# Kernel tuning notes

Hardware: AMD Instinct MI355X
Metric: run time of the kernel (lower is better)

The kernel has to match this reference:

```python
import jax, jax.numpy as jnp
import numpy as np

N_NODES = 50000
N_EDGES = 800000
LATENT = 128
HIDDEN = 256
N_NODE_TYPES = 32
N_EDGE_TYPES = 8


def setup_inputs() -> dict:
    key = jax.random.key(0)
    ks = jax.random.split(key, 8)
    z = jax.random.normal(ks[0], (N_NODES, LATENT), dtype=jnp.float32)
    edge_index = jax.random.randint(ks[1], (2, N_EDGES), 0, N_NODES, dtype=jnp.int64)
    # node_type_proj: Linear(latent, num_node_types)
    s_np = 1.0 / np.sqrt(LATENT)
    W_node = jax.random.uniform(ks[2], (LATENT, N_NODE_TYPES), minval=-s_np, maxval=s_np, dtype=jnp.float32)
    b_node = jax.random.uniform(ks[3], (N_NODE_TYPES,), minval=-s_np, maxval=s_np, dtype=jnp.float32)
    # edge_mlp: Linear(2*latent, hidden) -> ReLU -> Linear(hidden, num_edge_types)
    s1 = 1.0 / np.sqrt(2 * LATENT)
    W1 = jax.random.uniform(ks[4], (2 * LATENT, HIDDEN), minval=-s1, maxval=s1, dtype=jnp.float32)
    b1 = jax.random.uniform(ks[5], (HIDDEN,), minval=-s1, maxval=s1, dtype=jnp.float32)
    s2 = 1.0 / np.sqrt(HIDDEN)
    W2 = jax.random.uniform(ks[6], (HIDDEN, N_EDGE_TYPES), minval=-s2, maxval=s2, dtype=jnp.float32)
    b2 = jax.random.uniform(ks[7], (N_EDGE_TYPES,), minval=-s2, maxval=s2, dtype=jnp.float32)
    return {"z": z, "edge_index": edge_index, "W_node": W_node, "b_node": b_node,
            "W1": W1, "b1": b1, "W2": W2, "b2": b2}


def reference(z, edge_index, W_node, b_node, W1, b1, W2, b2):
    # node logits: [N, num_node_types]
    node_logits = z @ W_node + b_node
    row, col = edge_index[0], edge_index[1]
    # gather node pairs and concat: [E, 2*latent]
    edge_features = jnp.concatenate([z[row], z[col]], axis=-1)
    h = jax.nn.relu(edge_features @ W1 + b1)
    edge_logits = h @ W2 + b2  # [E, num_edge_types]
    return (node_logits, edge_logits)
```

## Files before the change

### kernel.cpp

```cpp
#include <hip/hip_runtime.h>
#include <hip/hip_bf16.h>
#include <stdint.h>

#define NNODES 50000
#define NEDGES 800000
#define LATENT 128
#define NTYPES 32
#define NTILES 25000
#define GRID_E 512

typedef __bf16 bf16x8 __attribute__((ext_vector_type(8)));
typedef float floatx4 __attribute__((ext_vector_type(4)));
typedef unsigned int u32;

#if defined(__has_builtin)
#if __has_builtin(__builtin_amdgcn_global_load_lds)
#define HAS_GLD_LDS 1
#endif
#endif

__device__ __forceinline__ void lds_barrier() {
    asm volatile("s_waitcnt lgkmcnt(0)\n\ts_barrier" ::: "memory");
}

__device__ __forceinline__ void gather16(const __hip_bfloat16* g, __hip_bfloat16* lbase, int lane) {
#ifdef HAS_GLD_LDS
    __builtin_amdgcn_global_load_lds(
        (const __attribute__((address_space(1))) u32*)(uintptr_t)g,
        (__attribute__((address_space(3))) u32*)(u32)(uintptr_t)lbase,
        16, 0, 0);
#else
    *(uint4*)(lbase + lane * 8) = *(const uint4*)g;
#endif
}

__device__ __forceinline__ int load_idx(const int* ei, bool i64, int half, size_t e) {
    size_t pos = (size_t)half * NEDGES + e;
    return i64 ? ei[2 * pos] : ei[pos];
}

__global__ __launch_bounds__(256) void transpose_kernel(
    const float* __restrict__ W1, const float* __restrict__ W2,
    __hip_bfloat16* __restrict__ W1T, __hip_bfloat16* __restrict__ W2Tp) {
    int n = blockIdx.x;
    int k = threadIdx.x;
    W1T[n * 256 + k] = __float2bfloat16(W1[k * 256 + n]);
    if (n < 16) {
        __hip_bfloat16 v = __float2bfloat16(n < 8 ? W2[k * 8 + n] : 0.f);
        W2Tp[n * 256 + k] = v;
    }
}

__global__ __launch_bounds__(256) void node_kernel(
    const float* __restrict__ z, const float* __restrict__ Wn,
    const float* __restrict__ bn, float* __restrict__ out,
    __hip_bfloat16* __restrict__ zbf) {
    __shared__ float wt[32][129];
    __shared__ float zl[8][128];
    int t = threadIdx.x;
#pragma unroll
    for (int i = 0; i < 16; ++i) {
        int flat = t + 256 * i;
        int k = flat >> 5, ty = flat & 31;
        wt[ty][k] = Wn[flat];
    }
    int node0 = blockIdx.x * 8;
    float4 v = ((const float4*)(z + (size_t)node0 * LATENT))[t];
    ((float4*)zl)[t] = v;
    {
        __hip_bfloat16 o[4];
        o[0] = __float2bfloat16(v.x); o[1] = __float2bfloat16(v.y);
        o[2] = __float2bfloat16(v.z); o[3] = __float2bfloat16(v.w);
        *(uint2*)&zbf[(size_t)node0 * LATENT + t * 4] = *(const uint2*)o;
    }
    __syncthreads();
    int ty = t & 31, ln = t >> 5;
    float acc = bn[ty];
#pragma unroll 16
    for (int k = 0; k < 128; ++k) acc += zl[ln][k] * wt[ty][k];
    out[(size_t)(node0 + ln) * NTYPES + ty] = acc;
}

#define W2T_ROW 264

__global__ __launch_bounds__(256, 2) void edge_kernel(
    const __hip_bfloat16* __restrict__ zbf, const int* __restrict__ ei,
    const __hip_bfloat16* __restrict__ W1T, const float* __restrict__ b1,
    const __hip_bfloat16* __restrict__ W2T, const float* __restrict__ b2,
    float* __restrict__ out) {
    __shared__ __align__(16) __hip_bfloat16 ef[2][32 * 256];
    __shared__ __align__(16) __hip_bfloat16 w2t[16 * W2T_ROW];
    __shared__ int idx_lds[2][64];

    int t = threadIdx.x;
    int lane = t & 63, wave = t >> 6;
    int l16 = lane & 15, quad = lane >> 4;
    int sw = l16 & 7;
    int nb = wave * 64;

    bool i64 = ((ei[1] | ei[3] | ei[5] | ei[7] | ei[9] | ei[11] | ei[13] | ei[15]) == 0);

    {
        const uint4* src = (const uint4*)W2T;
#pragma unroll
        for (int i = 0; i < 2; ++i) {
            int p = t + 256 * i;
            int n = p >> 5, c = p & 31;
            *(uint4*)&w2t[n * W2T_ROW + c * 8] = src[p];
        }
    }

    bf16x8 breg[4][8];
#pragma unroll
    for (int nt = 0; nt < 4; ++nt) {
        const __hip_bfloat16* rowp = W1T + (size_t)(nb + nt * 16 + l16) * 256 + quad * 8;
#pragma unroll
        for (int kt = 0; kt < 8; ++kt) breg[nt][kt] = *(const bf16x8*)(rowp + kt * 32);
    }

    floatx4 b1v[4];
#pragma unroll
    for (int nt = 0; nt < 4; ++nt)
        b1v[nt] = *(const floatx4*)&b1[nb + nt * 16 + quad * 4];
    float b2v = (l16 < 8) ? b2[l16] : 0.f;

    int tile = blockIdx.x;
    if (t < 64) idx_lds[0][t] = load_idx(ei, i64, t >> 5, (size_t)tile * 32 + (t & 31));
    __syncthreads();
    {
#pragma unroll
        for (int i = 0; i < 4; ++i) {
            int ii = wave * 4 + i;
            int s = ii * 64 + lane;
            int e = s >> 5, cp = s & 31;
            int c = cp ^ (e & 7);
            int node = idx_lds[0][(c >> 4) * 32 + e];
            gather16(zbf + (size_t)node * LATENT + (c & 15) * 8, &ef[0][ii * 512], lane);
        }
    }
    int v_idx = 0;
    {
        int t1 = tile + GRID_E; if (t1 >= NTILES) t1 = tile;
        if (t < 64) v_idx = load_idx(ei, i64, t >> 5, (size_t)t1 * 32 + (t & 31));
    }

    int cur = 0;
    for (; tile < NTILES; tile += GRID_E) {
        int nxt = cur ^ 1;
        if (t < 64) idx_lds[nxt][t] = v_idx;
        __syncthreads();

        {
#pragma unroll
            for (int i = 0; i < 4; ++i) {
                int ii = wave * 4 + i;
                int s = ii * 64 + lane;
                int e = s >> 5, cp = s & 31;
                int c = cp ^ (e & 7);
                int node = idx_lds[nxt][(c >> 4) * 32 + e];
                gather16(zbf + (size_t)node * LATENT + (c & 15) * 8, &ef[nxt][ii * 512], lane);
            }
        }
        {
            int t2 = tile + 2 * GRID_E; if (t2 >= NTILES) t2 = tile;
            if (t < 64) v_idx = load_idx(ei, i64, t >> 5, (size_t)t2 * 32 + (t & 31));
        }

        const __hip_bfloat16* efc = ef[cur];
        floatx4 acc[4][2];
#pragma unroll
        for (int a = 0; a < 4; ++a)
#pragma unroll
            for (int b = 0; b < 2; ++b) acc[a][b] = floatx4{0.f, 0.f, 0.f, 0.f};

#pragma unroll
        for (int kt = 0; kt < 8; ++kt) {
            bf16x8 bfrag[2];
#pragma unroll
            for (int et = 0; et < 2; ++et) {
                int e = et * 16 + l16;
                int chunk = e * 32 + ((kt * 4 + quad) ^ sw);
                bfrag[et] = *(const bf16x8*)&efc[chunk * 8];
            }
#pragma unroll
            for (int nt = 0; nt < 4; ++nt)
#pragma unroll
                for (int et = 0; et < 2; ++et)
                    acc[nt][et] = __builtin_amdgcn_mfma_f32_16x16x32_bf16(
                        breg[nt][kt], bfrag[et], acc[nt][et], 0, 0, 0);
        }

        lds_barrier();

        __hip_bfloat16* efh = ef[cur];
#pragma unroll
        for (int nt = 0; nt < 4; ++nt)
#pragma unroll
            for (int et = 0; et < 2; ++et) {
                __hip_bfloat16 pk[4];
#pragma unroll
                for (int r = 0; r < 4; ++r) {
                    float v = acc[nt][et][r] + b1v[nt][r];
                    pk[r] = __float2bfloat16(v > 0.f ? v : 0.f);
                }
                int e = et * 16 + l16;
                int hb = nb + nt * 16 + quad * 4;
                int phys = (hb >> 3) ^ (e & 7);
                *(uint2*)&efh[e * 256 + phys * 8 + (hb & 7)] = *(const uint2*)pk;
            }
        lds_barrier();

        if (wave < 2) {
            floatx4 acc2 = floatx4{0.f, 0.f, 0.f, 0.f};
#pragma unroll
            for (int kt = 0; kt < 8; ++kt) {
                int e = wave * 16 + l16;
                int chunk = e * 32 + ((kt * 4 + quad) ^ sw);
                bf16x8 a2 = *(const bf16x8*)&efc[chunk * 8];
                bf16x8 b2f = *(const bf16x8*)&w2t[l16 * W2T_ROW + (kt * 4 + quad) * 8];
                acc2 = __builtin_amdgcn_mfma_f32_16x16x32_bf16(a2, b2f, acc2, 0, 0, 0);
            }
            if (l16 < 8) {
                size_t e0 = (size_t)tile * 32;
#pragma unroll
                for (int r = 0; r < 4; ++r) {
                    size_t erow = e0 + wave * 16 + quad * 4 + r;
                    out[erow * 8 + l16] = acc2[r] + b2v;
                }
            }
        }
        cur ^= 1;
    }
}

extern "C" void kernel_launch(void* const* d_in, const int* in_sizes, int n_in,
                              void* d_out, int out_size, void* d_ws, size_t ws_size,
                              hipStream_t stream) {
    const float* z  = (const float*)d_in[0];
    const int* ei   = (const int*)d_in[1];
    const float* Wn = (const float*)d_in[2];
    const float* bn = (const float*)d_in[3];
    const float* W1 = (const float*)d_in[4];
    const float* b1 = (const float*)d_in[5];
    const float* W2 = (const float*)d_in[6];
    const float* b2 = (const float*)d_in[7];
    float* out = (float*)d_out;

    __hip_bfloat16* zbf  = (__hip_bfloat16*)d_ws;
    __hip_bfloat16* W1T  = zbf + (size_t)NNODES * LATENT;
    __hip_bfloat16* W2Tp = W1T + 256 * 256;

    hipLaunchKernelGGL(transpose_kernel, dim3(256), dim3(256), 0, stream, W1, W2, W1T, W2Tp);
    hipLaunchKernelGGL(node_kernel, dim3(NNODES / 8), dim3(256), 0, stream, z, Wn, bn, out, zbf);
    hipLaunchKernelGGL(edge_kernel, dim3(GRID_E), dim3(256), 0, stream,
                       zbf, ei, W1T, b1, W2Tp, b2, out + (size_t)NNODES * NTYPES);
}
```

Before: 214.2 us.

## Fuse weight transposes and node projection into one prep kernel; raise MFMA priority

Merges the W1/W2 transpose kernel and the node-logit kernel into a single launch whose blocks take different roles by block index, which removes one kernel launch. The node projection now handles 64 nodes per block with a 4x2 register tile per thread, so the W_node matrix is staged into LDS far fewer times. The W1 transpose goes through tiled LDS with coalesced reads and writes. It also wraps the edge kernel's MFMA loops in s_setprio so those waves get issue priority over waves doing gathers.

```diff
diff --git a/kernel.cpp b/kernel.cpp
--- a/kernel.cpp
+++ b/kernel.cpp
@@ -8,6 +8,9 @@
 #define NTYPES 32
 #define NTILES 25000
 #define GRID_E 512
+
+#define NODE_BLOCKS 782
+#define PREP_GRID (NODE_BLOCKS + 16 + 1)
 
 typedef __bf16 bf16x8 __attribute__((ext_vector_type(8)));
 typedef float floatx4 __attribute__((ext_vector_type(4)));
@@ -39,46 +42,98 @@
     return i64 ? ei[2 * pos] : ei[pos];
 }
 
-__global__ __launch_bounds__(256) void transpose_kernel(
+__global__ __launch_bounds__(256) void prep_kernel(
+    const float* __restrict__ z, const float* __restrict__ Wn, const float* __restrict__ bn,
     const float* __restrict__ W1, const float* __restrict__ W2,
+    float* __restrict__ out, __hip_bfloat16* __restrict__ zbf,
     __hip_bfloat16* __restrict__ W1T, __hip_bfloat16* __restrict__ W2Tp) {
-    int n = blockIdx.x;
-    int k = threadIdx.x;
-    W1T[n * 256 + k] = __float2bfloat16(W1[k * 256 + n]);
-    if (n < 16) {
-        __hip_bfloat16 v = __float2bfloat16(n < 8 ? W2[k * 8 + n] : 0.f);
-        W2Tp[n * 256 + k] = v;
-    }
-}
-
-__global__ __launch_bounds__(256) void node_kernel(
-    const float* __restrict__ z, const float* __restrict__ Wn,
-    const float* __restrict__ bn, float* __restrict__ out,
-    __hip_bfloat16* __restrict__ zbf) {
-    __shared__ float wt[32][129];
-    __shared__ float zl[8][128];
+    __shared__ __align__(16) float pool[96 * 129];
     int t = threadIdx.x;
-#pragma unroll
-    for (int i = 0; i < 16; ++i) {
-        int flat = t + 256 * i;
-        int k = flat >> 5, ty = flat & 31;
-        wt[ty][k] = Wn[flat];
-    }
-    int node0 = blockIdx.x * 8;
-    float4 v = ((const float4*)(z + (size_t)node0 * LATENT))[t];
-    ((float4*)zl)[t] = v;
-    {
-        __hip_bfloat16 o[4];
-        o[0] = __float2bfloat16(v.x); o[1] = __float2bfloat16(v.y);
-        o[2] = __float2bfloat16(v.z); o[3] = __float2bfloat16(v.w);
-        *(uint2*)&zbf[(size_t)node0 * LATENT + t * 4] = *(const uint2*)o;
-    }
-    __syncthreads();
-    int ty = t & 31, ln = t >> 5;
-    float acc = bn[ty];
+    int b = blockIdx.x;
+
+    if (b < NODE_BLOCKS) {
+        float* zl = pool;
+        float* wt = pool + 64 * 129;
+        int node0 = b * 64;
+#pragma unroll
+        for (int r = 0; r < 16; ++r) {
+            int idx = t + 256 * r;
+            wt[(idx & 31) * 129 + (idx >> 5)] = Wn[idx];
+        }
+#pragma unroll
+        for (int r = 0; r < 8; ++r) {
+            int idx = t + 256 * r;
+            int row = idx >> 5, c4 = idx & 31;
+            int node = node0 + row;
+            int srcn = node < NNODES ? node : (NNODES - 1);
+            float4 v = *(const float4*)&z[(size_t)srcn * LATENT + c4 * 4];
+            float* zp = zl + row * 129 + c4 * 4;
+            zp[0] = v.x; zp[1] = v.y; zp[2] = v.z; zp[3] = v.w;
+            if (node < NNODES) {
+                __hip_bfloat16 o[4];
+                o[0] = __float2bfloat16(v.x); o[1] = __float2bfloat16(v.y);
+                o[2] = __float2bfloat16(v.z); o[3] = __float2bfloat16(v.w);
+                *(uint2*)&zbf[(size_t)node * LATENT + c4 * 4] = *(const uint2*)o;
+            }
+        }
+        __syncthreads();
+        int ng = t & 15, tg = t >> 4;
+        const float* z0p = zl + (ng * 4 + 0) * 129;
+        const float* z1p = zl + (ng * 4 + 1) * 129;
+        const float* z2p = zl + (ng * 4 + 2) * 129;
+        const float* z3p = zl + (ng * 4 + 3) * 129;
+        const float* w0p = wt + (tg * 2 + 0) * 129;
+        const float* w1p = wt + (tg * 2 + 1) * 129;
+        float a00 = 0.f, a01 = 0.f, a10 = 0.f, a11 = 0.f;
+        float a20 = 0.f, a21 = 0.f, a30 = 0.f, a31 = 0.f;
 #pragma unroll 16
-    for (int k = 0; k < 128; ++k) acc += zl[ln][k] * wt[ty][k];
-    out[(size_t)(node0 + ln) * NTYPES + ty] = acc;
+        for (int k = 0; k < 128; ++k) {
+            float w0 = w0p[k], w1 = w1p[k];
+            float x0 = z0p[k], x1 = z1p[k], x2 = z2p[k], x3 = z3p[k];
+            a00 += x0 * w0; a01 += x0 * w1;
+            a10 += x1 * w0; a11 += x1 * w1;
+            a20 += x2 * w0; a21 += x2 * w1;
+            a30 += x3 * w0; a31 += x3 * w1;
+        }
+        float bb0 = bn[tg * 2], bb1 = bn[tg * 2 + 1];
+        float ar[4][2] = {{a00, a01}, {a10, a11}, {a20, a21}, {a30, a31}};
+#pragma unroll
+        for (int i = 0; i < 4; ++i) {
+            int node = node0 + ng * 4 + i;
+            if (node < NNODES) {
+                float2 o; o.x = ar[i][0] + bb0; o.y = ar[i][1] + bb1;
+                *(float2*)&out[(size_t)node * NTYPES + tg * 2] = o;
+            }
+        }
+    } else if (b < NODE_BLOCKS + 16) {
+        float* tl = pool;
+        int tb = b - NODE_BLOCKS, bi = tb >> 2, bj = tb & 3;
+#pragma unroll
+        for (int r = 0; r < 4; ++r) {
+            int idx = t + 256 * r;
+            int row = idx >> 4, c4 = idx & 15;
+            float4 v = *(const float4*)&W1[(size_t)(bi * 64 + row) * 256 + bj * 64 + c4 * 4];
+            float* tp = tl + row * 65 + c4 * 4;
+            tp[0] = v.x; tp[1] = v.y; tp[2] = v.z; tp[3] = v.w;
+        }
+        __syncthreads();
+#pragma unroll
+        for (int r = 0; r < 4; ++r) {
+            int idx = t + 256 * r;
+            int rr = idx >> 4, cq = idx & 15;
+            __hip_bfloat16 o[4];
+#pragma unroll
+            for (int s = 0; s < 4; ++s) o[s] = __float2bfloat16(tl[(cq * 4 + s) * 65 + rr]);
+            *(uint2*)&W1T[(size_t)(bj * 64 + rr) * 256 + bi * 64 + cq * 4] = *(const uint2*)o;
+        }
+    } else {
+#pragma unroll
+        for (int r = 0; r < 16; ++r) {
+            int idx = t + 256 * r;
+            int n = idx >> 8, k = idx & 255;
+            W2Tp[n * 256 + k] = __float2bfloat16(n < 8 ? W2[k * 8 + n] : 0.f);
+        }
+    }
 }
 
 #define W2T_ROW 264
@@ -173,6 +228,7 @@
 #pragma unroll
             for (int b = 0; b < 2; ++b) acc[a][b] = floatx4{0.f, 0.f, 0.f, 0.f};
 
+        __builtin_amdgcn_s_setprio(1);
 #pragma unroll
         for (int kt = 0; kt < 8; ++kt) {
             bf16x8 bfrag[2];
@@ -189,6 +245,7 @@
                     acc[nt][et] = __builtin_amdgcn_mfma_f32_16x16x32_bf16(
                         breg[nt][kt], bfrag[et], acc[nt][et], 0, 0, 0);
         }
+        __builtin_amdgcn_s_setprio(0);
 
         lds_barrier();
 
@@ -212,6 +269,7 @@
 
         if (wave < 2) {
             floatx4 acc2 = floatx4{0.f, 0.f, 0.f, 0.f};
+            __builtin_amdgcn_s_setprio(1);
 #pragma unroll
             for (int kt = 0; kt < 8; ++kt) {
                 int e = wave * 16 + l16;
@@ -220,6 +278,7 @@
                 bf16x8 b2f = *(const bf16x8*)&w2t[l16 * W2T_ROW + (kt * 4 + quad) * 8];
                 acc2 = __builtin_amdgcn_mfma_f32_16x16x32_bf16(a2, b2f, acc2, 0, 0, 0);
             }
+            __builtin_amdgcn_s_setprio(0);
             if (l16 < 8) {
                 size_t e0 = (size_t)tile * 32;
 #pragma unroll
@@ -250,8 +309,8 @@
     __hip_bfloat16* W1T  = zbf + (size_t)NNODES * LATENT;
     __hip_bfloat16* W2Tp = W1T + 256 * 256;
 
-    hipLaunchKernelGGL(transpose_kernel, dim3(256), dim3(256), 0, stream, W1, W2, W1T, W2Tp);
-    hipLaunchKernelGGL(node_kernel, dim3(NNODES / 8), dim3(256), 0, stream, z, Wn, bn, out, zbf);
+    hipLaunchKernelGGL(prep_kernel, dim3(PREP_GRID), dim3(256), 0, stream,
+                       z, Wn, bn, W1, W2, out, zbf, W1T, W2Tp);
     hipLaunchKernelGGL(edge_kernel, dim3(GRID_E), dim3(256), 0, stream,
                        zbf, ei, W1T, b1, W2Tp, b2, out + (size_t)NNODES * NTYPES);
 }
```

Result: no change. 212.7 us (-0.7%).
